# Optimization experiments

Hardware: AMD Instinct MI355X
Metric: run time of the kernel (lower is better)

The kernel has to match this reference:

```python
import jax, jax.numpy as jnp
import numpy as np

EMB = 16
N_LEFT = 200000
N_RIGHT = 200000
N_EDGES = 4000000


def _linear_params(key, out_dim, in_dim, bias=True):
    k1, k2 = jax.random.split(key)
    bound = 1.0 / np.sqrt(in_dim)
    W = jax.random.uniform(k1, (out_dim, in_dim), minval=-bound, maxval=bound, dtype=jnp.float32)
    if bias:
        b = jax.random.uniform(k2, (out_dim,), minval=-bound, maxval=bound, dtype=jnp.float32)
        return W, b
    return W


def setup_inputs() -> dict:
    key = jax.random.key(0)
    ks = jax.random.split(key, 12)
    left_features = jax.random.normal(ks[0], (N_LEFT, EMB), dtype=jnp.float32)
    right_features = jax.random.normal(ks[1], (N_RIGHT, EMB), dtype=jnp.float32)
    edge_features = jax.random.normal(ks[2], (N_EDGES, 1), dtype=jnp.float32)
    left_idx = jax.random.randint(ks[3], (N_EDGES,), 0, N_LEFT)
    right_idx = jax.random.randint(ks[4], (N_EDGES,), 0, N_RIGHT)
    edge_indices = jnp.stack([left_idx, right_idx], axis=0).astype(jnp.int64)

    W_left, b_left = _linear_params(ks[5], EMB, EMB, bias=True)
    W_edge = _linear_params(ks[6], EMB, 1, bias=False)
    W_right = _linear_params(ks[7], EMB, EMB, bias=False)
    W_final, b_final = _linear_params(ks[8], EMB, EMB, bias=True)
    W_post, b_post = _linear_params(ks[9], EMB, EMB, bias=True)
    W_out1, b_out1 = _linear_params(ks[10], EMB, 2 * EMB, bias=True)
    W_out2, b_out2 = _linear_params(ks[11], EMB, EMB, bias=True)

    return {
        "left_features": left_features,
        "edge_features": edge_features,
        "right_features": right_features,
        "edge_indices": edge_indices,
        "W_left": W_left, "b_left": b_left,
        "W_edge": W_edge,
        "W_right": W_right,
        "W_final": W_final, "b_final": b_final,
        "W_post": W_post, "b_post": b_post,
        "W_out1": W_out1, "b_out1": b_out1,
        "W_out2": W_out2, "b_out2": b_out2,
    }


def reference(left_features, edge_features, right_features, edge_indices,
              W_left, b_left, W_edge, W_right, W_final, b_final,
              W_post, b_post, W_out1, b_out1, W_out2, b_out2):
    n_right = right_features.shape[0]
    left_idx = edge_indices[0]
    right_idx = edge_indices[1]

    # per-edge message: Linear(left gathered) + edge Linear + Linear(right gathered)
    pre = (left_features[left_idx] @ W_left.T + b_left
           + edge_features @ W_edge.T
           + right_features[right_idx] @ W_right.T)  # [E, emb]
    msg = jax.nn.relu(pre) @ W_final.T + b_final     # fm_final: ReLU -> Linear

    # scatter-add aggregate per right node
    aggregated = jax.ops.segment_sum(msg, right_idx, num_segments=n_right)  # [n_right, emb]

    post = jax.nn.relu(aggregated) @ W_post.T + b_post  # post: ReLU -> Linear
    cat = jnp.concatenate([post, right_features], axis=-1)  # [n_right, 2*emb]
    h = jax.nn.relu(cat @ W_out1.T + b_out1)
    return h @ W_out2.T + b_out2
```

## Files before the change

kernel.cpp:

```cpp
#include <hip/hip_runtime.h>
#include <hip/hip_bf16.h>
#include <hip/hip_fp16.h>

#define EMB 16
#define EPT 4

typedef _Float16 half8 __attribute__((ext_vector_type(8)));
typedef _Float16 half2v __attribute__((ext_vector_type(2)));

#if defined(__has_builtin)
#if __has_builtin(__builtin_amdgcn_fdot2)
#define HAS_FDOT2 1
#endif
#endif

union U32H2 { int i; half2v h; };

__global__ __launch_bounds__(256) void node_transform2_kernel(
    const float* __restrict__ left, const float* __restrict__ right,
    const float* __restrict__ Wl, const float* __restrict__ bl,
    const float* __restrict__ Wr,
    _Float16* __restrict__ TL, _Float16* __restrict__ TR, int NL, int NR) {
    __shared__ float sWl[EMB * EMB], sWr[EMB * EMB], sbl[EMB];
    if (threadIdx.x < EMB * EMB) {
        sWl[threadIdx.x] = Wl[threadIdx.x];
        sWr[threadIdx.x] = Wr[threadIdx.x];
    }
    if (threadIdx.x < EMB) sbl[threadIdx.x] = bl[threadIdx.x];
    __syncthreads();

    int n = blockIdx.x * blockDim.x + threadIdx.x;
    if (n >= NL + NR) return;
    bool is_left = (n < NL);
    const float* X = is_left ? (left + (size_t)n * EMB)
                             : (right + (size_t)(n - NL) * EMB);
    _Float16* Y = is_left ? (TL + (size_t)n * EMB)
                          : (TR + (size_t)(n - NL) * EMB);
    const float* sW = is_left ? sWl : sWr;

    float x[EMB];
    const float4* xp = (const float4*)X;
    float4 x0 = xp[0], x1 = xp[1], x2 = xp[2], x3 = xp[3];
    x[0] = x0.x; x[1] = x0.y; x[2] = x0.z; x[3] = x0.w;
    x[4] = x1.x; x[5] = x1.y; x[6] = x1.z; x[7] = x1.w;
    x[8] = x2.x; x[9] = x2.y; x[10] = x2.z; x[11] = x2.w;
    x[12] = x3.x; x[13] = x3.y; x[14] = x3.z; x[15] = x3.w;

    float y[EMB];
#pragma unroll
    for (int j = 0; j < EMB; ++j) {
        float a = is_left ? sbl[j] : 0.0f;
#pragma unroll
        for (int k = 0; k < EMB; ++k) a = fmaf(sW[j * EMB + k], x[k], a);
        y[j] = a;
    }

    half8* yp = (half8*)Y;
    half8 h0, h1;
#pragma unroll
    for (int k = 0; k < 8; ++k) h0[k] = (_Float16)y[k];
#pragma unroll
    for (int k = 0; k < 8; ++k) h1[k] = (_Float16)y[8 + k];
    yp[0] = h0;
    yp[1] = h1;
}

__global__ __launch_bounds__(256) void edge_scatter_kernel(
    const int* __restrict__ idx, const float* __restrict__ ef,
    const _Float16* __restrict__ TL, const _Float16* __restrict__ TR,
    const float* __restrict__ wedge, const float* __restrict__ Wf,
    const float* __restrict__ bf, __half2* __restrict__ S, int E, int G) {
    int gid = blockIdx.x * blockDim.x + threadIdx.x;
    int g = gid >> 4;
    int t = gid & 15;

    int lane = threadIdx.x & 63;
    int gbase = lane & 48;
    int bp0 = (gbase | ((2 * t) & 15)) << 2;
    int bp1 = (gbase | ((2 * t + 1) & 15)) << 2;

    float we = wedge[t];
    float bft = bf[t];
    half2v wpk[8];
    {
        const float* wr = Wf + t * EMB;
#pragma unroll
        for (int k = 0; k < 8; ++k) {
            wpk[k][0] = (_Float16)wr[2 * k];
            wpk[k][1] = (_Float16)wr[2 * k + 1];
        }
    }

    int l[EPT], r[EPT];
    float efv[EPT];
    bool valid[EPT];
#pragma unroll
    for (int j = 0; j < EPT; ++j) {
        int e = g + j * G;
        valid[j] = (e < E);
        int ec = valid[j] ? e : 0;
        l[j] = idx[ec];
        r[j] = idx[E + ec];
        efv[j] = ef[ec];
    }

    _Float16 ah[EPT], bh[EPT];
#pragma unroll
    for (int j = 0; j < EPT; ++j) {
        ah[j] = TL[(size_t)l[j] * EMB + t];
        bh[j] = TR[(size_t)r[j] * EMB + t];
    }

    const bool odd = (t & 1);

#pragma unroll
    for (int j = 0; j < EPT; ++j) {
        float v = fmaxf((float)ah[j] + (float)bh[j] + efv[j] * we, 0.0f);

        int hvi = (int)__half_as_ushort(__float2half(v));
        int hxi = __builtin_amdgcn_ds_swizzle(hvi, 0x041F);
        int lo = odd ? hxi : hvi;
        int hi = odd ? hvi : hxi;
        int pk = (lo & 0xFFFF) | (hi << 16);

        float w = bft;
#define DOT_STEP(K)                                                           \
        {                                                                     \
            U32H2 u;                                                          \
            u.i = __builtin_amdgcn_ds_swizzle(pk, ((2 * (K)) << 5) | 0x10);   \
            DOT_BODY(K)                                                       \
        }
#if defined(HAS_FDOT2)
#define DOT_BODY(K) w = __builtin_amdgcn_fdot2(u.h, wpk[K], w, false);
#else
#define DOT_BODY(K)                                                           \
            w = fmaf((float)u.h[0], (float)wpk[K][0], w);                     \
            w = fmaf((float)u.h[1], (float)wpk[K][1], w);
#endif
        DOT_STEP(0) DOT_STEP(1) DOT_STEP(2) DOT_STEP(3)
        DOT_STEP(4) DOT_STEP(5) DOT_STEP(6) DOT_STEP(7)
#undef DOT_STEP
#undef DOT_BODY

        int wi = __float_as_int(w);
        float w0 = __int_as_float(__builtin_amdgcn_ds_bpermute(bp0, wi));
        float w1 = __int_as_float(__builtin_amdgcn_ds_bpermute(bp1, wi));
        if (valid[j] && t < 8) {
            __half2 hv = __floats2half2_rn(w0, w1);
            unsafeAtomicAdd(S + (size_t)r[j] * 8 + t, hv);
        }
    }
}

__global__ __launch_bounds__(256) void epilogue_kernel(
    const _Float16* __restrict__ S, const float* __restrict__ right,
    const float* __restrict__ Wp, const float* __restrict__ bp,
    const float* __restrict__ Wo1, const float* __restrict__ bo1,
    const float* __restrict__ Wo2, const float* __restrict__ bo2,
    float* __restrict__ out, int N) {
    __shared__ float sWp[256], sWo2[256], sWo1[512];
    __shared__ float sbp[16], sbo1[16], sbo2[16];
    for (int i = threadIdx.x; i < 256; i += blockDim.x) {
        sWp[i] = Wp[i]; sWo2[i] = Wo2[i];
    }
    for (int i = threadIdx.x; i < 512; i += blockDim.x) sWo1[i] = Wo1[i];
    if (threadIdx.x < 16) {
        sbp[threadIdx.x] = bp[threadIdx.x];
        sbo1[threadIdx.x] = bo1[threadIdx.x];
        sbo2[threadIdx.x] = bo2[threadIdx.x];
    }
    __syncthreads();

    int n = blockIdx.x * blockDim.x + threadIdx.x;
    if (n >= N) return;

    float ra[EMB];
    {
        const half8* sp = (const half8*)(S + (size_t)n * EMB);
        half8 a0 = sp[0], a1 = sp[1];
#pragma unroll
        for (int k = 0; k < 8; ++k) ra[k] = fmaxf((float)a0[k], 0.0f);
#pragma unroll
        for (int k = 0; k < 8; ++k) ra[8 + k] = fmaxf((float)a1[k], 0.0f);
    }

    float p[EMB];
#pragma unroll
    for (int j = 0; j < EMB; ++j) {
        float a = sbp[j];
#pragma unroll
        for (int k = 0; k < EMB; ++k) a = fmaf(sWp[j * EMB + k], ra[k], a);
        p[j] = a;
    }

    float rf[EMB];
    {
        const float4* rp = (const float4*)(right + (size_t)n * EMB);
        float4 a0 = rp[0], a1 = rp[1], a2 = rp[2], a3 = rp[3];
        rf[0] = a0.x; rf[1] = a0.y; rf[2] = a0.z; rf[3] = a0.w;
        rf[4] = a1.x; rf[5] = a1.y; rf[6] = a1.z; rf[7] = a1.w;
        rf[8] = a2.x; rf[9] = a2.y; rf[10] = a2.z; rf[11] = a2.w;
        rf[12] = a3.x; rf[13] = a3.y; rf[14] = a3.z; rf[15] = a3.w;
    }

    float h[EMB];
#pragma unroll
    for (int j = 0; j < EMB; ++j) {
        float a = sbo1[j];
#pragma unroll
        for (int k = 0; k < EMB; ++k) a = fmaf(sWo1[j * 32 + k], p[k], a);
#pragma unroll
        for (int k = 0; k < EMB; ++k) a = fmaf(sWo1[j * 32 + 16 + k], rf[k], a);
        h[j] = fmaxf(a, 0.0f);
    }

    float o[EMB];
#pragma unroll
    for (int j = 0; j < EMB; ++j) {
        float a = sbo2[j];
#pragma unroll
        for (int k = 0; k < EMB; ++k) a = fmaf(sWo2[j * EMB + k], h[k], a);
        o[j] = a;
    }

    float4* op = (float4*)(out + (size_t)n * EMB);
    op[0] = make_float4(o[0], o[1], o[2], o[3]);
    op[1] = make_float4(o[4], o[5], o[6], o[7]);
    op[2] = make_float4(o[8], o[9], o[10], o[11]);
    op[3] = make_float4(o[12], o[13], o[14], o[15]);
}

extern "C" void kernel_launch(void* const* d_in, const int* in_sizes, int n_in,
                              void* d_out, int out_size, void* d_ws, size_t ws_size,
                              hipStream_t stream) {
    const float* left  = (const float*)d_in[0];
    const float* ef    = (const float*)d_in[1];
    const float* right = (const float*)d_in[2];
    const int*   eidx  = (const int*)d_in[3];
    const float* W_left  = (const float*)d_in[4];
    const float* b_left  = (const float*)d_in[5];
    const float* W_edge  = (const float*)d_in[6];
    const float* W_right = (const float*)d_in[7];
    const float* W_final = (const float*)d_in[8];
    const float* b_final = (const float*)d_in[9];
    const float* W_post  = (const float*)d_in[10];
    const float* b_post  = (const float*)d_in[11];
    const float* W_out1  = (const float*)d_in[12];
    const float* b_out1  = (const float*)d_in[13];
    const float* W_out2  = (const float*)d_in[14];
    const float* b_out2  = (const float*)d_in[15];

    const int NL = in_sizes[0] / EMB;
    const int NR = in_sizes[2] / EMB;
    const int E  = in_sizes[1];

    size_t tl_b = (size_t)NL * EMB * 2;
    size_t tr_b = (size_t)NR * EMB * 2;
    char* ws = (char*)d_ws;
    _Float16* TL = (_Float16*)ws;
    _Float16* TR = (_Float16*)(ws + tl_b);
    _Float16* S16 = (_Float16*)(ws + tl_b + tr_b);

    (void)hipMemsetAsync(S16, 0, (size_t)NR * EMB * 2, stream);

    node_transform2_kernel<<<(NL + NR + 255) / 256, 256, 0, stream>>>(
        left, right, W_left, b_left, W_right, TL, TR, NL, NR);

    {
        int G = (E + EPT - 1) / EPT;
        long long threads = (long long)G * 16;
        int blocks = (int)((threads + 255) / 256);
        edge_scatter_kernel<<<blocks, 256, 0, stream>>>(
            eidx, ef, TL, TR, W_edge, W_final, b_final, (__half2*)S16, E, G);
    }

    epilogue_kernel<<<(NR + 255) / 256, 256, 0, stream>>>(
        S16, right, W_post, b_post, W_out1, b_out1, W_out2, b_out2,
        (float*)d_out, NR);
}
```

Measured before the change: 353.9 us.

## Fuse memset, node transform, edge scatter and epilogue into one cooperative kernel

Replaces the memset plus three kernel launches with a single persistent cooperative kernel that uses grid-wide syncs between the zeroing/node-transform, edge-scatter and epilogue phases. The edge phase processes eight edges per 16-lane group instead of four, and the grid is sized from the occupancy query. This aims to remove launch gaps and per-launch overhead, at the cost of two grid barriers, a fixed persistent grid that grid-strides over the work, and higher register pressure. If the cooperative launch fails, the old multi-kernel path is used.

```diff
diff --git a/kernel.cpp b/kernel.cpp
--- a/kernel.cpp
+++ b/kernel.cpp
@@ -1,9 +1,13 @@
 #include <hip/hip_runtime.h>
 #include <hip/hip_bf16.h>
 #include <hip/hip_fp16.h>
+#include <hip/hip_cooperative_groups.h>
+
+namespace cg = cooperative_groups;
 
 #define EMB 16
 #define EPT 4
+#define FEPT 8
 
 typedef _Float16 half8 __attribute__((ext_vector_type(8)));
 typedef _Float16 half2v __attribute__((ext_vector_type(2)));
@@ -15,6 +19,217 @@
 #endif
 
 union U32H2 { int i; half2v h; };
+
+struct FArgs {
+    const float* left; const float* ef; const float* right; const int* idx;
+    const float* Wl; const float* bl; const float* Wedge; const float* Wr;
+    const float* Wf; const float* bf; const float* Wp; const float* bp;
+    const float* Wo1; const float* bo1; const float* Wo2; const float* bo2;
+    _Float16* TL; _Float16* TR; _Float16* S16; float* out;
+    int NL, NR, E, G;
+};
+
+__global__ __launch_bounds__(256, 4) void fused_kernel(FArgs a) {
+    cg::grid_group grid = cg::this_grid();
+    const int tid = threadIdx.x;
+    const int gtid = blockIdx.x * 256 + tid;
+    const int nthreads = gridDim.x * 256;
+
+    __shared__ float sWl[256], sWr[256], sbl[16];
+    __shared__ float sWp[256], sWo2[256], sWo1[512];
+    __shared__ float sbp[16], sbo1[16], sbo2[16];
+
+    {
+        uint4* Sz = (uint4*)a.S16;
+        const uint4 z = make_uint4(0u, 0u, 0u, 0u);
+        int n4 = a.NR * 2;
+        for (int i = gtid; i < n4; i += nthreads) Sz[i] = z;
+    }
+
+    if (tid < 256) { sWl[tid] = a.Wl[tid]; sWr[tid] = a.Wr[tid]; }
+    if (tid < 16) sbl[tid] = a.bl[tid];
+    __syncthreads();
+
+    for (int n = gtid; n < a.NL + a.NR; n += nthreads) {
+        bool is_left = (n < a.NL);
+        const float* X = is_left ? (a.left + (size_t)n * EMB)
+                                 : (a.right + (size_t)(n - a.NL) * EMB);
+        _Float16* Y = is_left ? (a.TL + (size_t)n * EMB)
+                              : (a.TR + (size_t)(n - a.NL) * EMB);
+        const float* sW = is_left ? sWl : sWr;
+
+        float x[EMB];
+        const float4* xp = (const float4*)X;
+        float4 x0 = xp[0], x1 = xp[1], x2 = xp[2], x3 = xp[3];
+        x[0] = x0.x; x[1] = x0.y; x[2] = x0.z; x[3] = x0.w;
+        x[4] = x1.x; x[5] = x1.y; x[6] = x1.z; x[7] = x1.w;
+        x[8] = x2.x; x[9] = x2.y; x[10] = x2.z; x[11] = x2.w;
+        x[12] = x3.x; x[13] = x3.y; x[14] = x3.z; x[15] = x3.w;
+
+        float y[EMB];
+#pragma unroll
+        for (int j = 0; j < EMB; ++j) {
+            float acc = is_left ? sbl[j] : 0.0f;
+#pragma unroll
+            for (int k = 0; k < EMB; ++k) acc = fmaf(sW[j * EMB + k], x[k], acc);
+            y[j] = acc;
+        }
+        half8 h0, h1;
+#pragma unroll
+        for (int k = 0; k < 8; ++k) h0[k] = (_Float16)y[k];
+#pragma unroll
+        for (int k = 0; k < 8; ++k) h1[k] = (_Float16)y[8 + k];
+        ((half8*)Y)[0] = h0;
+        ((half8*)Y)[1] = h1;
+    }
+
+    grid.sync();
+
+    {
+        const int t = tid & 15;
+        const int lane = tid & 63;
+        const int gbase = lane & 48;
+        const int bp0 = (gbase | ((2 * t) & 15)) << 2;
+        const int bp1 = (gbase | ((2 * t + 1) & 15)) << 2;
+
+        const float we = a.Wedge[t];
+        const float bft = a.bf[t];
+        half2v wpk[8];
+        {
+            const float* wr = a.Wf + t * EMB;
+#pragma unroll
+            for (int k = 0; k < 8; ++k) {
+                wpk[k][0] = (_Float16)wr[2 * k];
+                wpk[k][1] = (_Float16)wr[2 * k + 1];
+            }
+        }
+        const bool odd = (t & 1);
+        const int G = a.G;
+        const int NG = nthreads >> 4;
+        __half2* S = (__half2*)a.S16;
+
+        for (int g = gtid >> 4; g < G; g += NG) {
+            int l[FEPT], r[FEPT];
+            float efv[FEPT];
+            bool valid[FEPT];
+#pragma unroll
+            for (int j = 0; j < FEPT; ++j) {
+                int e = g + j * G;
+                valid[j] = (e < a.E);
+                int ec = valid[j] ? e : 0;
+                l[j] = a.idx[ec];
+                r[j] = a.idx[a.E + ec];
+                efv[j] = a.ef[ec];
+            }
+            _Float16 ah[FEPT], bh[FEPT];
+#pragma unroll
+            for (int j = 0; j < FEPT; ++j) {
+                ah[j] = a.TL[(size_t)l[j] * EMB + t];
+                bh[j] = a.TR[(size_t)r[j] * EMB + t];
+            }
+#pragma unroll
+            for (int j = 0; j < FEPT; ++j) {
+                float v = fmaxf((float)ah[j] + (float)bh[j] + efv[j] * we, 0.0f);
+
+                int hvi = (int)__half_as_ushort(__float2half(v));
+                int hxi = __builtin_amdgcn_ds_swizzle(hvi, 0x041F);
+                int lo = odd ? hxi : hvi;
+                int hi = odd ? hvi : hxi;
+                int pk = (lo & 0xFFFF) | (hi << 16);
+
+                float w = bft;
+#define DOT_STEP(K)                                                           \
+                {                                                             \
+                    U32H2 u;                                                  \
+                    u.i = __builtin_amdgcn_ds_swizzle(                        \
+                        pk, ((2 * (K)) << 5) | 0x10);                         \
+                    DOT_BODY(K)                                               \
+                }
+#if defined(HAS_FDOT2)
+#define DOT_BODY(K) w = __builtin_amdgcn_fdot2(u.h, wpk[K], w, false);
+#else
+#define DOT_BODY(K)                                                           \
+                    w = fmaf((float)u.h[0], (float)wpk[K][0], w);             \
+                    w = fmaf((float)u.h[1], (float)wpk[K][1], w);
+#endif
+                DOT_STEP(0) DOT_STEP(1) DOT_STEP(2) DOT_STEP(3)
+                DOT_STEP(4) DOT_STEP(5) DOT_STEP(6) DOT_STEP(7)
+#undef DOT_STEP
+#undef DOT_BODY
+
+                int wi = __float_as_int(w);
+                float w0 = __int_as_float(__builtin_amdgcn_ds_bpermute(bp0, wi));
+                float w1 = __int_as_float(__builtin_amdgcn_ds_bpermute(bp1, wi));
+                if (valid[j] && t < 8) {
+                    __half2 hv = __floats2half2_rn(w0, w1);
+                    unsafeAtomicAdd(S + (size_t)r[j] * 8 + t, hv);
+                }
+            }
+        }
+    }
+
+    grid.sync();
+
+    for (int i = tid; i < 256; i += 256) { sWp[i] = a.Wp[i]; sWo2[i] = a.Wo2[i]; }
+    for (int i = tid; i < 512; i += 256) sWo1[i] = a.Wo1[i];
+    if (tid < 16) {
+        sbp[tid] = a.bp[tid]; sbo1[tid] = a.bo1[tid]; sbo2[tid] = a.bo2[tid];
+    }
+    __syncthreads();
+
+    for (int n = gtid; n < a.NR; n += nthreads) {
+        float ra[EMB];
+        {
+            const half8* sp = (const half8*)(a.S16 + (size_t)n * EMB);
+            half8 a0 = sp[0], a1 = sp[1];
+#pragma unroll
+            for (int k = 0; k < 8; ++k) ra[k] = fmaxf((float)a0[k], 0.0f);
+#pragma unroll
+            for (int k = 0; k < 8; ++k) ra[8 + k] = fmaxf((float)a1[k], 0.0f);
+        }
+        float p[EMB];
+#pragma unroll
+        for (int j = 0; j < EMB; ++j) {
+            float acc = sbp[j];
+#pragma unroll
+            for (int k = 0; k < EMB; ++k) acc = fmaf(sWp[j * EMB + k], ra[k], acc);
+            p[j] = acc;
+        }
+        float rf[EMB];
+        {
+            const float4* rp = (const float4*)(a.right + (size_t)n * EMB);
+            float4 a0 = rp[0], a1 = rp[1], a2 = rp[2], a3 = rp[3];
+            rf[0] = a0.x; rf[1] = a0.y; rf[2] = a0.z; rf[3] = a0.w;
+            rf[4] = a1.x; rf[5] = a1.y; rf[6] = a1.z; rf[7] = a1.w;
+            rf[8] = a2.x; rf[9] = a2.y; rf[10] = a2.z; rf[11] = a2.w;
+            rf[12] = a3.x; rf[13] = a3.y; rf[14] = a3.z; rf[15] = a3.w;
+        }
+        float h[EMB];
+#pragma unroll
+        for (int j = 0; j < EMB; ++j) {
+            float acc = sbo1[j];
+#pragma unroll
+            for (int k = 0; k < EMB; ++k) acc = fmaf(sWo1[j * 32 + k], p[k], acc);
+#pragma unroll
+            for (int k = 0; k < EMB; ++k)
+                acc = fmaf(sWo1[j * 32 + 16 + k], rf[k], acc);
+            h[j] = fmaxf(acc, 0.0f);
+        }
+        float o[EMB];
+#pragma unroll
+        for (int j = 0; j < EMB; ++j) {
+            float acc = sbo2[j];
+#pragma unroll
+            for (int k = 0; k < EMB; ++k) acc = fmaf(sWo2[j * EMB + k], h[k], acc);
+            o[j] = acc;
+        }
+        float4* op = (float4*)(a.out + (size_t)n * EMB);
+        op[0] = make_float4(o[0], o[1], o[2], o[3]);
+        op[1] = make_float4(o[4], o[5], o[6], o[7]);
+        op[2] = make_float4(o[8], o[9], o[10], o[11]);
+        op[3] = make_float4(o[12], o[13], o[14], o[15]);
+    }
+}
 
 __global__ __launch_bounds__(256) void node_transform2_kernel(
     const float* __restrict__ left, const float* __restrict__ right,
@@ -116,7 +331,6 @@
 #pragma unroll
     for (int j = 0; j < EPT; ++j) {
         float v = fmaxf((float)ah[j] + (float)bh[j] + efv[j] * we, 0.0f);
-
         int hvi = (int)__half_as_ushort(__float2half(v));
         int hxi = __builtin_amdgcn_ds_swizzle(hvi, 0x041F);
         int lo = odd ? hxi : hvi;
@@ -261,6 +475,28 @@
     _Float16* TR = (_Float16*)(ws + tl_b);
     _Float16* S16 = (_Float16*)(ws + tl_b + tr_b);
 
+    FArgs args;
+    args.left = left; args.ef = ef; args.right = right; args.idx = eidx;
+    args.Wl = W_left; args.bl = b_left; args.Wedge = W_edge; args.Wr = W_right;
+    args.Wf = W_final; args.bf = b_final; args.Wp = W_post; args.bp = b_post;
+    args.Wo1 = W_out1; args.bo1 = b_out1; args.Wo2 = W_out2; args.bo2 = b_out2;
+    args.TL = TL; args.TR = TR; args.S16 = S16; args.out = (float*)d_out;
+    args.NL = NL; args.NR = NR; args.E = E;
+    args.G = (E + FEPT - 1) / FEPT;
+
+    int maxB = 0;
+    hipError_t qe = hipOccupancyMaxActiveBlocksPerMultiprocessor(
+        &maxB, (const void*)fused_kernel, 256, 0);
+    if (qe != hipSuccess || maxB < 1) maxB = 3;
+    if (maxB > 8) maxB = 8;
+    int blocks = 256 * maxB;
+
+    void* kparams[] = {(void*)&args};
+    hipError_t le = hipLaunchCooperativeKernel(
+        (const void*)fused_kernel, dim3(blocks), dim3(256), kparams, 0, stream);
+
+    if (le == hipSuccess) return;
+
     (void)hipMemsetAsync(S16, 0, (size_t)NR * EMB * 2, stream);
 
     node_transform2_kernel<<<(NL + NR + 255) / 256, 256, 0, stream>>>(
@@ -269,8 +505,8 @@
     {
         int G = (E + EPT - 1) / EPT;
         long long threads = (long long)G * 16;
-        int blocks = (int)((threads + 255) / 256);
-        edge_scatter_kernel<<<blocks, 256, 0, stream>>>(
+        int nblocks = (int)((threads + 255) / 256);
+        edge_scatter_kernel<<<nblocks, 256, 0, stream>>>(
             eidx, ef, TL, TR, W_edge, W_final, b_final, (__half2*)S16, E, G);
     }
 
```

Result: slower. 743.6 us (+110.1%).
